# Performance work log

Hardware: AMD Instinct MI355X
Metric: run time of the kernel (lower is better)

The kernel has to match this reference:

```python
import jax, jax.numpy as jnp
import numpy as np

EMBED_DIM = 1024


def setup_inputs() -> dict:
    key = jax.random.key(0)
    ks = jax.random.split(key, 9)
    d = EMBED_DIM
    s = 1.0 / np.sqrt(d)
    x = jax.random.normal(ks[0], (4, 2048, d), dtype=jnp.float32)
    # nn.Linear weights are [out, in]; we store them transposed for x @ W
    Wq = jax.random.uniform(ks[1], (d, d), jnp.float32, -s, s)
    bq = jax.random.uniform(ks[2], (d,), jnp.float32, -s, s)
    Wk = jax.random.uniform(ks[3], (d, d), jnp.float32, -s, s)
    bk = jax.random.uniform(ks[4], (d,), jnp.float32, -s, s)
    Wv = jax.random.uniform(ks[5], (d, d), jnp.float32, -s, s)
    bv = jax.random.uniform(ks[6], (d,), jnp.float32, -s, s)
    Wo = jax.random.uniform(ks[7], (d, d), jnp.float32, -s, s)
    bo = jax.random.uniform(ks[8], (d,), jnp.float32, -s, s)
    return {"x": x, "Wq": Wq, "bq": bq, "Wk": Wk, "bk": bk,
            "Wv": Wv, "bv": bv, "Wo": Wo, "bo": bo}


def reference(x, Wq, bq, Wk, bk, Wv, bv, Wo, bo):
    b, seq_len, d = x.shape
    scaling = 1.0 / jnp.sqrt(jnp.float32(d))
    q = x @ Wq + bq  # [b, s, d]
    k = x @ Wk + bk
    v = x @ Wv + bv
    scores = jnp.einsum('bqd,bkd->bqk', q, k) * scaling  # [b, s, s]
    causal = jnp.tril(jnp.ones((seq_len, seq_len), dtype=bool))
    scores = jnp.where(causal, scores, -jnp.inf)
    attn = jax.nn.softmax(scores, axis=-1)
    out = jnp.einsum('bqk,bkd->bqd', attn, v)
    return out @ Wo + bo
```

## Files before the change

### kernel.cpp

```cpp
#include <hip/hip_runtime.h>
#include <stdint.h>

typedef __bf16 bf16_t;
typedef __bf16 bf16x8 __attribute__((ext_vector_type(8)));
typedef __bf16 bf16x4 __attribute__((ext_vector_type(4)));
typedef float  f32x4  __attribute__((ext_vector_type(4)));

#define DEV __device__ __forceinline__

constexpr int S = 2048, D = 1024, BATCH = 4, MF = BATCH * S;

DEV void gload16(const void* g, void* l) {
  __builtin_amdgcn_global_load_lds(
      (const __attribute__((address_space(1))) void*)g,
      (__attribute__((address_space(3))) void*)(uint32_t)(uintptr_t)l,
      16, 0, 0);
}

template<int EP>
__global__ __launch_bounds__(256, 2) void gemm_core(
    const bf16_t* __restrict__ A, const bf16_t* __restrict__ B,
    void* __restrict__ C0, void* __restrict__ C1, void* __restrict__ C2,
    const float* __restrict__ aux, float* __restrict__ part,
    int M, int N, int K, long sA, long sB)
{
  const int tm = blockIdx.x, tn = blockIdx.y, bz = blockIdx.z;
  if (EP == 2 && tn > tm) return;
  const int m0 = tm * 128, n0 = tn * 128;
  int kmax = K;
  if (EP == 3) { int t = m0 + 128; kmax = t < K ? t : K; }
  A += (long)bz * sA;
  B += (long)bz * sB;

  __shared__ __align__(16) bf16_t ldsA[128 * 64];
  __shared__ __align__(16) bf16_t ldsB[128 * 64];

  const int tid  = threadIdx.x;
  const int lane = tid & 63;
  const int wave = tid >> 6;
  const int wm = wave & 1, wn = wave >> 1;
  const int l8r = lane >> 3;
  const int swz = ((lane & 7) ^ (lane >> 3)) * 8;
  const int cl  = lane & 15;
  const int qd  = lane >> 4;
  const int ch0 = ((qd ^ (cl & 7)) * 8);

  f32x4 acc[4][4] = {};

  for (int k0 = 0; k0 < kmax; k0 += 64) {
    #pragma unroll
    for (int t = 0; t < 4; ++t) {
      const int rb = wave * 4 + t;
      gload16(A + (long)(m0 + rb * 8 + l8r) * K + (k0 + swz), &ldsA[rb * 512]);
      gload16(B + (long)(n0 + rb * 8 + l8r) * K + (k0 + swz), &ldsB[rb * 512]);
    }
    __syncthreads();
    #pragma unroll
    for (int kk = 0; kk < 64; kk += 32) {
      bf16x8 af[4], bg[4];
      #pragma unroll
      for (int i = 0; i < 4; ++i)
        af[i] = *(const bf16x8*)&ldsA[(wm * 64 + i * 16 + cl) * 64 + (ch0 ^ kk)];
      #pragma unroll
      for (int j = 0; j < 4; ++j)
        bg[j] = *(const bf16x8*)&ldsB[(wn * 64 + j * 16 + cl) * 64 + (ch0 ^ kk)];
      #pragma unroll
      for (int i = 0; i < 4; ++i)
        #pragma unroll
        for (int j = 0; j < 4; ++j)
          acc[i][j] = __builtin_amdgcn_mfma_f32_16x16x32_bf16(af[i], bg[j], acc[i][j], 0, 0, 0);
    }
    __syncthreads();
  }

  #pragma unroll
  for (int i = 0; i < 4; ++i) {
    const int gm0 = m0 + wm * 64 + i * 16 + qd * 4;

    if (EP == 0) {
      float* Co = (float*)C0;
      #pragma unroll
      for (int j = 0; j < 4; ++j) {
        const int gn = n0 + wn * 64 + j * 16 + cl;
        const float bn = aux[gn];
        #pragma unroll
        for (int r = 0; r < 4; ++r)
          Co[(long)(gm0 + r) * D + gn] = acc[i][j][r] + bn;
      }
    }

    if (EP == 1) {
      bf16_t* q  = (bf16_t*)C0;
      bf16_t* k  = (bf16_t*)C1;
      bf16_t* vT = (bf16_t*)C2;
      #pragma unroll
      for (int j = 0; j < 4; ++j) {
        const int gn  = n0 + wn * 64 + j * 16 + cl;
        const int sec = gn >> 10, ln = gn & 1023;
        const float bn = aux[gn];
        if (sec == 2) {
          const int z = gm0 >> 11, s0 = gm0 & 2047;
          bf16x4 v4;
          #pragma unroll
          for (int r = 0; r < 4; ++r) v4[r] = (bf16_t)(acc[i][j][r] + bn);
          *(bf16x4*)&vT[((long)z * D + ln) * S + s0] = v4;
        } else {
          bf16_t* dst = (sec == 0) ? q : k;
          #pragma unroll
          for (int r = 0; r < 4; ++r)
            dst[(long)(gm0 + r) * D + ln] = (bf16_t)(acc[i][j][r] + bn);
        }
      }
    }

    if (EP == 2) {
      bf16_t* probs = (bf16_t*)C0 + (long)bz * S * S;
      float ls[4] = {0.f, 0.f, 0.f, 0.f};
      #pragma unroll
      for (int j = 0; j < 4; ++j) {
        const int gn = n0 + wn * 64 + j * 16 + cl;
        #pragma unroll
        for (int r = 0; r < 4; ++r) {
          const int gm = gm0 + r;
          const float e = (gn <= gm) ? __expf(acc[i][j][r] * 0.03125f) : 0.0f;
          probs[(long)gm * S + gn] = (bf16_t)e;
          ls[r] += e;
        }
      }
      #pragma unroll
      for (int r = 0; r < 4; ++r) {
        float v = ls[r];
        v += __shfl_xor(v, 1); v += __shfl_xor(v, 2);
        v += __shfl_xor(v, 4); v += __shfl_xor(v, 8);
        if (cl == 0)
          part[((long)bz * S + (gm0 + r)) * 32 + tn * 2 + wn] = v;
      }
    }

    if (EP == 3) {
      bf16_t* attn = (bf16_t*)C0 + (long)bz * S * D;
      const float* invl = aux + (long)bz * S;
      float scl[4];
      #pragma unroll
      for (int r = 0; r < 4; ++r) scl[r] = invl[gm0 + r];
      #pragma unroll
      for (int j = 0; j < 4; ++j) {
        const int gn = n0 + wn * 64 + j * 16 + cl;
        #pragma unroll
        for (int r = 0; r < 4; ++r)
          attn[(long)(gm0 + r) * D + gn] = (bf16_t)(acc[i][j][r] * scl[r]);
      }
    }
  }
}

__global__ __launch_bounds__(256) void reduce_invl(
    const float* __restrict__ part, float* __restrict__ invl)
{
  const int r = blockIdx.x * 256 + threadIdx.x;
  const int row = r & (S - 1);
  const int cnt = ((row >> 7) + 1) * 2;
  const float* p = part + (long)r * 32;
  float s = 0.f;
  for (int j = 0; j < cnt; ++j) s += p[j];
  invl[r] = 1.0f / s;
}

__global__ __launch_bounds__(256) void cvt_x(
    const float4* __restrict__ in, bf16x4* __restrict__ out, int n4)
{
  const int i = blockIdx.x * 256 + threadIdx.x;
  if (i >= n4) return;
  float4 f = in[i];
  bf16x4 o;
  o.x = (__bf16)f.x; o.y = (__bf16)f.y; o.z = (__bf16)f.z; o.w = (__bf16)f.w;
  out[i] = o;
}

__global__ __launch_bounds__(256) void cvt_w_t(
    const float* __restrict__ W, bf16_t* __restrict__ WT)
{
  __shared__ float t[32][33];
  const int bx = blockIdx.x, by = blockIdx.y;
  const int tx = threadIdx.x & 31, ty = threadIdx.x >> 5;
  #pragma unroll
  for (int dy = 0; dy < 32; dy += 8)
    t[ty + dy][tx] = W[(long)(by * 32 + ty + dy) * 1024 + bx * 32 + tx];
  __syncthreads();
  #pragma unroll
  for (int dy = 0; dy < 32; dy += 8)
    WT[(long)(bx * 32 + ty + dy) * 1024 + by * 32 + tx] = (bf16_t)t[tx][ty + dy];
}

extern "C" void kernel_launch(void* const* d_in, const int* in_sizes, int n_in,
                              void* d_out, int out_size, void* d_ws, size_t ws_size,
                              hipStream_t stream) {
  const float* x  = (const float*)d_in[0];
  const float* Wq = (const float*)d_in[1];
  const float* bq = (const float*)d_in[2];
  const float* Wk = (const float*)d_in[3];
  const float* bk = (const float*)d_in[4];
  const float* Wv = (const float*)d_in[5];
  const float* bv = (const float*)d_in[6];
  const float* Wo = (const float*)d_in[7];
  const float* bo = (const float*)d_in[8];
  float* out = (float*)d_out;

  size_t off = 0;
  auto alloc = [&](size_t bytes) -> void* {
    void* p = (char*)d_ws + off;
    off += (bytes + 255) & ~(size_t)255;
    return p;
  };
  bf16_t* x_b   = (bf16_t*)alloc((size_t)MF * D * 2);
  bf16_t* WqkvT = (bf16_t*)alloc((size_t)3 * D * D * 2);
  bf16_t* WoT   = (bf16_t*)alloc((size_t)D * D * 2);
  float*  bqkv  = (float*) alloc((size_t)3 * D * 4);
  bf16_t* q_b   = (bf16_t*)alloc((size_t)MF * D * 2);
  bf16_t* k_b   = (bf16_t*)alloc((size_t)MF * D * 2);
  bf16_t* vT_b  = (bf16_t*)alloc((size_t)BATCH * D * S * 2);
  bf16_t* probs = (bf16_t*)alloc((size_t)BATCH * S * S * 2);
  float*  part  = (float*) alloc((size_t)MF * 32 * 4);
  float*  invl  = (float*) alloc((size_t)MF * 4);
  bf16_t* attn  = (bf16_t*)alloc((size_t)MF * D * 2);

  hipMemcpyAsync(bqkv,            bq, D * 4, hipMemcpyDeviceToDevice, stream);
  hipMemcpyAsync(bqkv + D,        bk, D * 4, hipMemcpyDeviceToDevice, stream);
  hipMemcpyAsync(bqkv + 2 * D,    bv, D * 4, hipMemcpyDeviceToDevice, stream);

  cvt_x<<<dim3((MF * D / 4 + 255) / 256), 256, 0, stream>>>(
      (const float4*)x, (bf16x4*)x_b, MF * D / 4);
  cvt_w_t<<<dim3(32, 32), 256, 0, stream>>>(Wq, WqkvT);
  cvt_w_t<<<dim3(32, 32), 256, 0, stream>>>(Wk, WqkvT + (size_t)D * D);
  cvt_w_t<<<dim3(32, 32), 256, 0, stream>>>(Wv, WqkvT + (size_t)2 * D * D);
  cvt_w_t<<<dim3(32, 32), 256, 0, stream>>>(Wo, WoT);

  gemm_core<1><<<dim3(MF / 128, 3 * D / 128, 1), 256, 0, stream>>>(
      x_b, WqkvT, q_b, k_b, vT_b, bqkv, nullptr, MF, 3 * D, D, 0, 0);

  gemm_core<2><<<dim3(S / 128, S / 128, BATCH), 256, 0, stream>>>(
      q_b, k_b, probs, nullptr, nullptr, nullptr, part,
      S, S, D, (long)S * D, (long)S * D);

  reduce_invl<<<dim3(MF / 256), 256, 0, stream>>>(part, invl);

  gemm_core<3><<<dim3(S / 128, D / 128, BATCH), 256, 0, stream>>>(
      probs, vT_b, attn, nullptr, nullptr, invl, nullptr,
      S, D, S, (long)S * S, (long)D * S);

  gemm_core<0><<<dim3(MF / 128, D / 128, 1), 256, 0, stream>>>(
      attn, WoT, out, nullptr, nullptr, bo, nullptr, MF, D, D, 0, 0);
}
```

Baseline: 285.3 us.

## Compact causal score grid, reverse PV order, batch weight converts, raise occupancy

The QK^T score kernel now launches only the 136 lower-triangular tiles per batch and maps each linear block index to a (row, col) tile through a triangular-root calculation, instead of launching the full square grid and returning early. The PV kernel walks row tiles in reverse so the longest causal tiles are scheduled first. The four weight transpose-converts become one launch, and three device-to-device bias memcpys become a small kernel, cutting launch overhead. Launch bounds rise to four blocks per CU, which may force register spilling given the 64 f32 accumulators per thread.

```diff
diff --git a/kernel.cpp b/kernel.cpp
--- a/kernel.cpp
+++ b/kernel.cpp
@@ -18,14 +18,22 @@
 }
 
 template<int EP>
-__global__ __launch_bounds__(256, 2) void gemm_core(
+__global__ __launch_bounds__(256, 4) void gemm_core(
     const bf16_t* __restrict__ A, const bf16_t* __restrict__ B,
     void* __restrict__ C0, void* __restrict__ C1, void* __restrict__ C2,
     const float* __restrict__ aux, float* __restrict__ part,
     int M, int N, int K, long sA, long sB)
 {
-  const int tm = blockIdx.x, tn = blockIdx.y, bz = blockIdx.z;
-  if (EP == 2 && tn > tm) return;
+  int tm = blockIdx.x, tn = blockIdx.y;
+  const int bz = blockIdx.z;
+  if (EP == 2) {
+    const int t = blockIdx.x;
+    tm = (int)((sqrtf(8.0f * t + 1.0f) - 1.0f) * 0.5f);
+    while ((tm + 1) * (tm + 2) / 2 <= t) ++tm;
+    while (tm * (tm + 1) / 2 > t) --tm;
+    tn = t - tm * (tm + 1) / 2;
+  }
+  if (EP == 3) tm = (int)gridDim.x - 1 - blockIdx.x;
   const int m0 = tm * 128, n0 = tn * 128;
   int kmax = K;
   if (EP == 3) { int t = m0 + 128; kmax = t < K ? t : K; }
@@ -177,9 +185,14 @@
   out[i] = o;
 }
 
-__global__ __launch_bounds__(256) void cvt_w_t(
-    const float* __restrict__ W, bf16_t* __restrict__ WT)
-{
+__global__ __launch_bounds__(256) void cvt_w_t4(
+    const float* __restrict__ W0, const float* __restrict__ W1,
+    const float* __restrict__ W2, const float* __restrict__ W3,
+    bf16_t* __restrict__ dst)
+{
+  const float* W = (blockIdx.z == 0) ? W0 : (blockIdx.z == 1) ? W1
+                 : (blockIdx.z == 2) ? W2 : W3;
+  bf16_t* WT = dst + (size_t)blockIdx.z * D * D;
   __shared__ float t[32][33];
   const int bx = blockIdx.x, by = blockIdx.y;
   const int tx = threadIdx.x & 31, ty = threadIdx.x >> 5;
@@ -190,6 +203,15 @@
   #pragma unroll
   for (int dy = 0; dy < 32; dy += 8)
     WT[(long)(bx * 32 + ty + dy) * 1024 + by * 32 + tx] = (bf16_t)t[tx][ty + dy];
+}
+
+__global__ __launch_bounds__(256) void stack_bias(
+    const float* __restrict__ bq, const float* __restrict__ bk,
+    const float* __restrict__ bv, float* __restrict__ o)
+{
+  const int i = blockIdx.x * 256 + threadIdx.x;
+  const float* s = (i < 1024) ? bq : (i < 2048) ? bk : bv;
+  o[i] = s[i & 1023];
 }
 
 extern "C" void kernel_launch(void* const* d_in, const int* in_sizes, int n_in,
@@ -213,8 +235,7 @@
     return p;
   };
   bf16_t* x_b   = (bf16_t*)alloc((size_t)MF * D * 2);
-  bf16_t* WqkvT = (bf16_t*)alloc((size_t)3 * D * D * 2);
-  bf16_t* WoT   = (bf16_t*)alloc((size_t)D * D * 2);
+  bf16_t* Wall  = (bf16_t*)alloc((size_t)4 * D * D * 2);
   float*  bqkv  = (float*) alloc((size_t)3 * D * 4);
   bf16_t* q_b   = (bf16_t*)alloc((size_t)MF * D * 2);
   bf16_t* k_b   = (bf16_t*)alloc((size_t)MF * D * 2);
@@ -223,22 +244,18 @@
   float*  part  = (float*) alloc((size_t)MF * 32 * 4);
   float*  invl  = (float*) alloc((size_t)MF * 4);
   bf16_t* attn  = (bf16_t*)alloc((size_t)MF * D * 2);
-
-  hipMemcpyAsync(bqkv,            bq, D * 4, hipMemcpyDeviceToDevice, stream);
-  hipMemcpyAsync(bqkv + D,        bk, D * 4, hipMemcpyDeviceToDevice, stream);
-  hipMemcpyAsync(bqkv + 2 * D,    bv, D * 4, hipMemcpyDeviceToDevice, stream);
+  bf16_t* WqkvT = Wall;
+  bf16_t* WoT   = Wall + (size_t)3 * D * D;
 
   cvt_x<<<dim3((MF * D / 4 + 255) / 256), 256, 0, stream>>>(
       (const float4*)x, (bf16x4*)x_b, MF * D / 4);
-  cvt_w_t<<<dim3(32, 32), 256, 0, stream>>>(Wq, WqkvT);
-  cvt_w_t<<<dim3(32, 32), 256, 0, stream>>>(Wk, WqkvT + (size_t)D * D);
-  cvt_w_t<<<dim3(32, 32), 256, 0, stream>>>(Wv, WqkvT + (size_t)2 * D * D);
-  cvt_w_t<<<dim3(32, 32), 256, 0, stream>>>(Wo, WoT);
+  cvt_w_t4<<<dim3(32, 32, 4), 256, 0, stream>>>(Wq, Wk, Wv, Wo, Wall);
+  stack_bias<<<dim3(12), 256, 0, stream>>>(bq, bk, bv, bqkv);
 
   gemm_core<1><<<dim3(MF / 128, 3 * D / 128, 1), 256, 0, stream>>>(
       x_b, WqkvT, q_b, k_b, vT_b, bqkv, nullptr, MF, 3 * D, D, 0, 0);
 
-  gemm_core<2><<<dim3(S / 128, S / 128, BATCH), 256, 0, stream>>>(
+  gemm_core<2><<<dim3(136, 1, BATCH), 256, 0, stream>>>(
       q_b, k_b, probs, nullptr, nullptr, nullptr, part,
       S, S, D, (long)S * D, (long)S * D);
 
```

New measurement: 280.1 us. Within noise of the previous version (-1.8%).
